# Kernel tuning notes

Hardware: AMD Instinct MI355X
Metric: run time of the kernel (lower is better)

The kernel has to match this reference:

```python
import jax, jax.numpy as jnp
import numpy as np

B, S, D = 4, 512, 4096
H, G = 32, 8           # num_heads, num_groups (GQA)
HD = D // H            # head_dim = 128
REP = H // G           # query heads per kv group = 4


def rotate_half(x):
    x1, x2 = x[..., : x.shape[-1] // 2], x[..., x.shape[-1] // 2 :]
    return jnp.concatenate([-x2, x1], axis=-1)


def setup_inputs() -> dict:
    key = jax.random.key(0)
    ks = jax.random.split(key, 5)
    return {
        "x": jax.random.normal(ks[0], (B, S, D), dtype=jnp.float32),
        "wq": jax.random.normal(ks[1], (D, D), dtype=jnp.float32) * 0.02,
        "bq": jnp.zeros((D,), dtype=jnp.float32),
        "wk": jax.random.normal(ks[2], (D, G * HD), dtype=jnp.float32) * 0.02,
        "bk": jnp.zeros((G * HD,), dtype=jnp.float32),
        "wv": jax.random.normal(ks[3], (D, G * HD), dtype=jnp.float32) * 0.02,
        "bv": jnp.zeros((G * HD,), dtype=jnp.float32),
        "wo": jax.random.normal(ks[4], (D, D), dtype=jnp.float32) * 0.02,
        "bo": jnp.zeros((D,), dtype=jnp.float32),
    }


def reference(x, wq, bq, wk, bk, wv, bv, wo, bo):
    b, s, d = x.shape
    q = (x @ wq + bq).reshape(b, s, H, HD)
    k = (x @ wk + bk).reshape(b, s, G, HD)
    v = (x @ wv + bv).reshape(b, s, G, HD)

    # RoPE tables (identical to module's cached sin/cos, sliced to seq len)
    inv_freq = 1.0 / (10000.0 ** (jnp.arange(0, HD, 2, dtype=jnp.float32) / HD))
    freqs = jnp.outer(jnp.arange(s, dtype=jnp.float32), inv_freq)  # [s, HD/2]
    freqs = jnp.concatenate([freqs, freqs], axis=-1)               # [s, HD]
    sin = jnp.sin(freqs)[:, None, :]  # [s, 1, HD] broadcast over heads
    cos = jnp.cos(freqs)[:, None, :]

    q = q * cos + rotate_half(q) * sin
    k = k * cos + rotate_half(k) * sin

    # Module scales q by HD**-0.5 AND jax.nn.dot_product_attention applies its
    # own default 1/sqrt(HD) -> net logit scale is HD**-1. Reproduce exactly.
    scale = HD ** (-0.5)
    q = q * scale

    # GQA without materializing repeated k/v: group query heads.
    qg = q.reshape(b, s, G, REP, HD)
    logits = jnp.einsum("bqgrd,bkgd->bgrqk", qg, k) * scale  # second scale (SDPA default)
    attn = jax.nn.softmax(logits, axis=-1)
    out = jnp.einsum("bgrqk,bkgd->bqgrd", attn, v).reshape(b, s, d)
    return out @ wo + bo
```

## Files before the change

kernel.cpp:

```cpp
#include <hip/hip_runtime.h>
#include <math.h>

typedef unsigned short ushort_t;
typedef __attribute__((ext_vector_type(8))) short bf16x8;
typedef __attribute__((ext_vector_type(4))) float f32x4;
typedef __attribute__((ext_vector_type(4))) unsigned short us4;
typedef __attribute__((ext_vector_type(8))) unsigned short us8;

#define B_   4
#define S_   512
#define D_   4096
#define H_   32
#define G_   8
#define HD_  128
#define KV_  1024
#define M_   (B_ * S_)
#define QN_  6144

__device__ __forceinline__ float bf2f(ushort_t u) {
    union { unsigned u; float f; } x; x.u = ((unsigned)u) << 16; return x.f;
}
__device__ __forceinline__ ushort_t f2bf(float f) {
    union { float f; unsigned u; } x; x.f = f;
    unsigned r = x.u + 0x7fffu + ((x.u >> 16) & 1u);
    return (ushort_t)(r >> 16);
}

typedef const __attribute__((address_space(1))) void* gptr_t;
typedef __attribute__((address_space(3))) void* ldsptr_t;

__device__ __forceinline__ void gload_lds16(const void* g, void* lds) {
    __builtin_amdgcn_global_load_lds((gptr_t)g, (ldsptr_t)lds, 16, 0, 0);
}

#define BAR() asm volatile("s_barrier" ::: "memory")
#define LGKM0() do { asm volatile("s_waitcnt lgkmcnt(0)" ::: "memory"); \
                     __builtin_amdgcn_sched_barrier(0); } while (0)

__global__ void xconv(const float* __restrict__ x, ushort_t* __restrict__ xb, int n8)
{
    const int i = blockIdx.x * blockDim.x + threadIdx.x;
    if (i >= n8) return;
    const float4 a = *(const float4*)&x[(size_t)i * 8];
    const float4 b = *(const float4*)&x[(size_t)i * 8 + 4];
    us8 o;
    o[0] = f2bf(a.x); o[1] = f2bf(a.y); o[2] = f2bf(a.z); o[3] = f2bf(a.w);
    o[4] = f2bf(b.x); o[5] = f2bf(b.y); o[6] = f2bf(b.z); o[7] = f2bf(b.w);
    *(us8*)&xb[(size_t)i * 8] = o;
}

__global__ __launch_bounds__(256) void wconv(
    const float* __restrict__ W, ushort_t* __restrict__ Wt, int K, int N)
{
    __shared__ float t[32][33];
    const int n0 = blockIdx.x * 32, k0 = blockIdx.y * 32;
    const int tid = threadIdx.x;
    const int r = tid >> 3, c4 = (tid & 7) * 4;
    const float4 v = *(const float4*)&W[(size_t)(k0 + r) * N + n0 + c4];
    t[r][c4 + 0] = v.x; t[r][c4 + 1] = v.y; t[r][c4 + 2] = v.z; t[r][c4 + 3] = v.w;
    __syncthreads();
    us4 o;
    o.x = f2bf(t[c4 + 0][r]);
    o.y = f2bf(t[c4 + 1][r]);
    o.z = f2bf(t[c4 + 2][r]);
    o.w = f2bf(t[c4 + 3][r]);
    *(us4*)&Wt[(size_t)(n0 + r) * K + k0 + c4] = o;
}

template<int OUT_BF16, int SPLITK>
__global__ __launch_bounds__(512, 2) void gemm8(
    const ushort_t* __restrict__ A, int lda,
    const ushort_t* __restrict__ Bt, int ldb,
    const float* __restrict__ bias0, const float* __restrict__ bias1,
    const float* __restrict__ bias2,
    float* __restrict__ Cf, ushort_t* __restrict__ Cb,
    float* __restrict__ P0, float* __restrict__ P1,
    int M, int N, int K)
{
    __shared__ ushort_t sA[2][256 * 64];
    __shared__ ushort_t sB[2][256 * 64];

    const int tid = threadIdx.x;
    const int lane = tid & 63, w = tid >> 6;
    const int lr = lane & 15, kg = lane >> 4;
    const int wr = w >> 2, wc = w & 3;

    const int nwg = gridDim.x;
    const int cpx = nwg >> 3;
    const int bid = (blockIdx.x & 7) * cpx + (blockIdx.x >> 3);
    int khalf = 0, tile = bid;
    if (SPLITK) { khalf = bid >> 7; tile = bid & 127; }
    const int nbx = N >> 8;
    const int bx = tile % nbx, by = tile / nbx;
    const int bm0 = by << 8, bn0 = bx << 8;
    if (SPLITK) { A += (size_t)khalf * K; Bt += (size_t)khalf * K; }

    const int NT = K >> 6;

    auto stage = [&](int t, int h) {
        const int c = t & 1;
        const ushort_t* gb; int ld; char* sbase;
        if (h < 2) { gb = A + (size_t)bm0 * lda; ld = lda; sbase = (char*)sA; }
        else       { gb = Bt + (size_t)bn0 * ldb; ld = ldb; sbase = (char*)sB; }
        const int half = h & 1;
        #pragma unroll
        for (int j = 0; j < 2; ++j) {
            const int o = j * 8192 + tid * 16;
            const int row = half * 128 + (o >> 7);
            const int slot = (o >> 4) & 7;
            gload_lds16(gb + (size_t)row * ld + t * 64 + ((slot ^ (row & 7)) << 3),
                        sbase + c * 32768 + half * 16384 + j * 8192 + w * 1024);
        }
    };
    auto lda_frag = [&](int c, int mi, int s) {
        const int row = mi * 32 + wr * 16 + lr;
        return *(const bf16x8*)((const char*)sA + c * 32768 + row * 128 +
                                (((s * 4 + kg) ^ (row & 7)) << 4));
    };
    auto ldb_frag = [&](int c, int ni, int s) {
        const int row = ni * 64 + wc * 16 + lr;
        return *(const bf16x8*)((const char*)sB + c * 32768 + row * 128 +
                                (((s * 4 + kg) ^ (row & 7)) << 4));
    };

    f32x4 acc[8][4];
    #pragma unroll
    for (int i = 0; i < 8; ++i)
        #pragma unroll
        for (int j = 0; j < 4; ++j)
            acc[i][j] = (f32x4){0.f, 0.f, 0.f, 0.f};

    stage(0, 0); stage(0, 2); stage(0, 3); stage(0, 1);
    stage(1, 0); stage(1, 2); stage(1, 3);
    asm volatile("s_waitcnt vmcnt(6)" ::: "memory");
    BAR();

    for (int t = 0; t < NT; ++t) {
        const int c = t & 1;
        bf16x8 a[4][2], b[4][2];

        #pragma unroll
        for (int mi = 0; mi < 4; ++mi)
            #pragma unroll
            for (int s = 0; s < 2; ++s) a[mi][s] = lda_frag(c, mi, s);
        #pragma unroll
        for (int ni = 0; ni < 2; ++ni)
            #pragma unroll
            for (int s = 0; s < 2; ++s) b[ni][s] = ldb_frag(c, ni, s);
        if (t + 1 < NT) stage(t + 1, 1);
        BAR();
        LGKM0();
        __builtin_amdgcn_s_setprio(1);
        #pragma unroll
        for (int mi = 0; mi < 4; ++mi)
            #pragma unroll
            for (int ni = 0; ni < 2; ++ni)
                #pragma unroll
                for (int s = 0; s < 2; ++s)
                    acc[mi][ni] = __builtin_amdgcn_mfma_f32_16x16x32_bf16(
                        a[mi][s], b[ni][s], acc[mi][ni], 0, 0, 0);
        __builtin_amdgcn_s_setprio(0);
        BAR();

        #pragma unroll
        for (int ni = 2; ni < 4; ++ni)
            #pragma unroll
            for (int s = 0; s < 2; ++s) b[ni][s] = ldb_frag(c, ni, s);
        if (t + 2 < NT) stage(t + 2, 0);
        BAR();
        LGKM0();
        __builtin_amdgcn_s_setprio(1);
        #pragma unroll
        for (int mi = 0; mi < 4; ++mi)
            #pragma unroll
            for (int ni = 2; ni < 4; ++ni)
                #pragma unroll
                for (int s = 0; s < 2; ++s)
                    acc[mi][ni] = __builtin_amdgcn_mfma_f32_16x16x32_bf16(
                        a[mi][s], b[ni][s], acc[mi][ni], 0, 0, 0);
        __builtin_amdgcn_s_setprio(0);
        BAR();

        #pragma unroll
        for (int mi = 0; mi < 4; ++mi)
            #pragma unroll
            for (int s = 0; s < 2; ++s) a[mi][s] = lda_frag(c, mi + 4, s);
        if (t + 2 < NT) stage(t + 2, 2);
        BAR();
        LGKM0();
        __builtin_amdgcn_s_setprio(1);
        #pragma unroll
        for (int mi = 0; mi < 4; ++mi)
            #pragma unroll
            for (int ni = 2; ni < 4; ++ni)
                #pragma unroll
                for (int s = 0; s < 2; ++s)
                    acc[mi + 4][ni] = __builtin_amdgcn_mfma_f32_16x16x32_bf16(
                        a[mi][s], b[ni][s], acc[mi + 4][ni], 0, 0, 0);
        __builtin_amdgcn_s_setprio(0);
        BAR();

        if (t + 2 < NT) {
            stage(t + 2, 3);
            asm volatile("s_waitcnt vmcnt(6)" ::: "memory");
        } else {
            asm volatile("s_waitcnt vmcnt(0)" ::: "memory");
        }
        BAR();
        __builtin_amdgcn_s_setprio(1);
        #pragma unroll
        for (int mi = 0; mi < 4; ++mi)
            #pragma unroll
            for (int ni = 0; ni < 2; ++ni)
                #pragma unroll
                for (int s = 0; s < 2; ++s)
                    acc[mi + 4][ni] = __builtin_amdgcn_mfma_f32_16x16x32_bf16(
                        a[mi][s], b[ni][s], acc[mi + 4][ni], 0, 0, 0);
        __builtin_amdgcn_s_setprio(0);
        BAR();
    }

    #pragma unroll
    for (int mi = 0; mi < 8; ++mi) {
        #pragma unroll
        for (int ni = 0; ni < 4; ++ni) {
            const int n = bn0 + ni * 64 + wc * 16 + lr;
            const float bs = (n < 4096) ? bias0[n]
                           : (n < 5120) ? bias1[n - 4096] : bias2[n - 5120];
            const int mr = bm0 + mi * 32 + wr * 16 + kg * 4;
            #pragma unroll
            for (int r = 0; r < 4; ++r) {
                if (SPLITK) {
                    const int row = mr + r;
                    if (khalf == 0) {
                        Cf[(size_t)row * N + n] = acc[mi][ni][r] + bs;
                    } else {
                        float* P = (row < 1024) ? P0 : P1;
                        P[((size_t)(row & 1023) << 12) + n] = acc[mi][ni][r];
                    }
                } else {
                    const float val = acc[mi][ni][r] + bs;
                    if (OUT_BF16) Cb[(size_t)(mr + r) * N + n] = f2bf(val);
                    else          Cf[(size_t)(mr + r) * N + n] = val;
                }
            }
        }
    }
}

__global__ void reduce_add(const float* __restrict__ P0, const float* __restrict__ P1,
                           float* __restrict__ out)
{
    const int i4 = blockIdx.x * blockDim.x + threadIdx.x;
    if (i4 >= M_ * D_ / 4) return;
    const float4 p = (i4 < (1 << 20))
        ? *(const float4*)&P0[(size_t)i4 * 4]
        : *(const float4*)&P1[(size_t)(i4 - (1 << 20)) * 4];
    float4 o = *(float4*)&out[(size_t)i4 * 4];
    o.x += p.x; o.y += p.y; o.z += p.z; o.w += p.w;
    *(float4*)&out[(size_t)i4 * 4] = o;
}

__global__ void rope_bf16(ushort_t* __restrict__ buf, int nh, float scale)
{
    const int i = blockIdx.x * blockDim.x + threadIdx.x;
    const int total = B_ * S_ * nh * 64;
    if (i >= total) return;
    const int j     = i & 63;
    const int t2    = i >> 6;
    const int head  = t2 % nh;
    const int token = t2 / nh;
    const int s     = token % S_;
    const size_t base = (size_t)token * QN_ + head * HD_;
    const float inv = __expf(-9.210340371976184f * (2.f * j) / (float)HD_);
    const float ang = (float)s * inv;
    float sn, cs;
    __sincosf(ang, &sn, &cs);
    const float x1 = bf2f(buf[base + j]);
    const float x2 = bf2f(buf[base + j + 64]);
    buf[base + j]      = f2bf((x1 * cs - x2 * sn) * scale);
    buf[base + j + 64] = f2bf((x2 * cs + x1 * sn) * scale);
}

__global__ __launch_bounds__(256) void vtrans(
    const ushort_t* __restrict__ vb,
    ushort_t* __restrict__ vT)
{
    __shared__ ushort_t t[32][40];
    const int s0 = blockIdx.x * 32;
    const int d0 = blockIdx.y * 32;
    const int bg = blockIdx.z;
    const int b = bg >> 3, g = bg & 7;
    const int tid = threadIdx.x;
    const int row = tid >> 3, c4 = (tid & 7) * 4;
    const us4 v = *(const us4*)&vb[(size_t)(b * S_ + s0 + row) * QN_ + g * HD_ + d0 + c4];
    t[row][c4 + 0] = v.x; t[row][c4 + 1] = v.y;
    t[row][c4 + 2] = v.z; t[row][c4 + 3] = v.w;
    __syncthreads();
    us4 o;
    o.x = t[c4 + 0][row]; o.y = t[c4 + 1][row];
    o.z = t[c4 + 2][row]; o.w = t[c4 + 3][row];
    *(us4*)&vT[(size_t)(bg * HD_ + d0 + row) * S_ + s0 + c4] = o;
}

__global__ __launch_bounds__(256) void attn_mfma(
    const ushort_t* __restrict__ kb,
    const ushort_t* __restrict__ vT,
    ushort_t* __restrict__ qb)
{
    __shared__ ushort_t sKV[8192];
    __shared__ ushort_t sP[4 * 16 * 512];

    const int q0 = blockIdx.x * 64;
    const int h = blockIdx.y, b = blockIdx.z;
    const int g = h >> 2;
    const int tid = threadIdx.x;
    const int lane = tid & 63, w = tid >> 6;
    const int lr = lane & 15, kg = lane >> 4;

    bf16x8 af[4];
    {
        const ushort_t* qrow = qb + (size_t)(b * S_ + q0 + w * 16 + lr) * QN_ + h * HD_;
        #pragma unroll
        for (int c = 0; c < 4; ++c)
            af[c] = *(const bf16x8*)(qrow + c * 32 + kg * 8);
    }

    f32x4 l[8][4];
    #pragma unroll
    for (int ch = 0; ch < 8; ++ch)
        #pragma unroll
        for (int t = 0; t < 4; ++t)
            l[ch][t] = (f32x4){0.f, 0.f, 0.f, 0.f};

    const ushort_t* kbase = kb + (size_t)b * S_ * QN_ + g * HD_;
    #pragma unroll
    for (int ch = 0; ch < 8; ++ch) {
        __syncthreads();
        #pragma unroll
        for (int i = 0; i < 4; ++i) {
            const int o = w * 4096 + i * 1024;
            const int key = (o >> 8) + (lane >> 4);
            const int sl = lane & 15;
            gload_lds16(kbase + (size_t)(ch * 64 + key) * QN_ + ((sl ^ (key & 15)) * 8),
                        (char*)sKV + o);
        }
        __syncthreads();
        #pragma unroll
        for (int t = 0; t < 4; ++t) {
            const int key = t * 16 + lr;
            #pragma unroll
            for (int c = 0; c < 4; ++c) {
                const bf16x8 bf = *(const bf16x8*)((const char*)sKV + key * 256 +
                                                   (((c * 4 + kg) ^ (key & 15)) << 4));
                l[ch][t] = __builtin_amdgcn_mfma_f32_16x16x32_bf16(af[c], bf, l[ch][t], 0, 0, 0);
            }
        }
    }

    float inv[4];
    #pragma unroll
    for (int r = 0; r < 4; ++r) {
        float m = -1e30f;
        #pragma unroll
        for (int ch = 0; ch < 8; ++ch)
            #pragma unroll
            for (int t = 0; t < 4; ++t)
                m = fmaxf(m, l[ch][t][r]);
        #pragma unroll
        for (int msk = 1; msk <= 8; msk <<= 1)
            m = fmaxf(m, __shfl_xor(m, msk));
        float s = 0.f;
        const int q = kg * 4 + r;
        #pragma unroll
        for (int ch = 0; ch < 8; ++ch)
            #pragma unroll
            for (int t = 0; t < 4; ++t) {
                const float p = __expf(l[ch][t][r] - m);
                s += p;
                const int gs = ch * 8 + t * 2 + (lr >> 3);
                sP[w * 8192 + q * 512 + ((gs ^ q) << 3) + (lr & 7)] = f2bf(p);
            }
        #pragma unroll
        for (int msk = 1; msk <= 8; msk <<= 1)
            s += __shfl_xor(s, msk);
        inv[r] = 1.f / s;
    }

    f32x4 oacc[8];
    #pragma unroll
    for (int dt = 0; dt < 8; ++dt) oacc[dt] = (f32x4){0.f, 0.f, 0.f, 0.f};

    const ushort_t* vbase = vT + (size_t)(b * G_ + g) * HD_ * S_;
    for (int ch = 0; ch < 8; ++ch) {
        __syncthreads();
        #pragma unroll
        for (int i = 0; i < 4; ++i) {
            const int o = w * 4096 + i * 1024;
            const int d = (o >> 7) + (lane >> 3);
            const int sl = lane & 7;
            gload_lds16(vbase + (size_t)d * S_ + ch * 64 + ((sl ^ (d & 7)) * 8),
                        (char*)sKV + o);
        }
        __syncthreads();
        #pragma unroll
        for (int c2 = 0; c2 < 2; ++c2) {
            const int gs = ch * 8 + c2 * 4 + kg;
            const bf16x8 ap = *(const bf16x8*)((const char*)sP + w * 16384 + lr * 1024 +
                                               ((gs ^ lr) << 4));
            #pragma unroll
            for (int dt = 0; dt < 8; ++dt) {
                const int d = dt * 16 + lr;
                const bf16x8 bv = *(const bf16x8*)((const char*)sKV + d * 128 +
                                                   (((c2 * 4 + kg) ^ (d & 7)) << 4));
                oacc[dt] = __builtin_amdgcn_mfma_f32_16x16x32_bf16(ap, bv, oacc[dt], 0, 0, 0);
            }
        }
    }

    #pragma unroll
    for (int dt = 0; dt < 8; ++dt) {
        #pragma unroll
        for (int r = 0; r < 4; ++r) {
            const int q = kg * 4 + r;
            qb[(size_t)(b * S_ + q0 + w * 16 + q) * QN_ + h * HD_ + dt * 16 + lr] =
                f2bf(oacc[dt][r] * inv[r]);
        }
    }
}

extern "C" void kernel_launch(void* const* d_in, const int* in_sizes, int n_in,
                              void* d_out, int out_size, void* d_ws, size_t ws_size,
                              hipStream_t stream)
{
    const float* x  = (const float*)d_in[0];
    const float* wq = (const float*)d_in[1];
    const float* bq = (const float*)d_in[2];
    const float* wk = (const float*)d_in[3];
    const float* bk = (const float*)d_in[4];
    const float* wv = (const float*)d_in[5];
    const float* bv = (const float*)d_in[6];
    const float* wo = (const float*)d_in[7];
    const float* bo = (const float*)d_in[8];
    float* out = (float*)d_out;

    char* ws = (char*)d_ws;
    ushort_t* xb   = (ushort_t*)(ws);
    ushort_t* Wt   = (ushort_t*)(ws + (16u << 20));
    ushort_t* vT   = (ushort_t*)(ws + (48u << 20));
    ushort_t* qkv  = (ushort_t*)(ws + (64u << 20));
    float* p0      = (float*)xb;
    float* p1      = (float*)(ws + (48u << 20));

    wconv<<<dim3(D_ / 32, D_ / 32), 256, 0, stream>>>(wq, Wt, D_, D_);
    wconv<<<dim3(KV_ / 32, D_ / 32), 256, 0, stream>>>(wk, Wt + (size_t)4096 * 4096, D_, KV_);
    wconv<<<dim3(KV_ / 32, D_ / 32), 256, 0, stream>>>(wv, Wt + (size_t)5120 * 4096, D_, KV_);
    xconv<<<(M_ * D_ / 8 + 255) / 256, 256, 0, stream>>>(x, xb, M_ * D_ / 8);

    gemm8<1, 0><<<(QN_ / 256) * (M_ / 256), 512, 0, stream>>>(
        xb, D_, Wt, D_, bq, bk, bv, nullptr, qkv, nullptr, nullptr, M_, QN_, D_);

    vtrans<<<dim3(S_ / 32, HD_ / 32, B_ * G_), 256, 0, stream>>>(qkv + 5120, vT);

    rope_bf16<<<(B_ * S_ * H_ * 64 + 255) / 256, 256, 0, stream>>>(qkv, H_, 1.f / 128.f);
    rope_bf16<<<(B_ * S_ * G_ * 64 + 255) / 256, 256, 0, stream>>>(qkv + 4096, G_, 1.f);

    attn_mfma<<<dim3(S_ / 64, H_, B_), 256, 0, stream>>>(qkv + 4096, vT, qkv);

    wconv<<<dim3(D_ / 32, D_ / 32), 256, 0, stream>>>(wo, Wt, D_, D_);

    gemm8<0, 1><<<256, 512, 0, stream>>>(
        qkv, QN_, Wt, D_, bo, bo, bo, out, nullptr, p0, p1, M_, D_, 2048);
    reduce_add<<<(M_ * D_ / 4 + 255) / 256, 256, 0, stream>>>(p0, p1, out);
}
```

Before: 327.0 us.

## Fuse RoPE into QKV GEMM epilogue and merge weight conversion launches

Applies rotary embedding and the q scaling directly in the QKV GEMM epilogue by pairing accumulator fragments 64 columns apart. This removes the two standalone rope kernels and their extra read-modify-write of q and k. The three weight-transpose conversions are merged into one launch, and reduce_add becomes a grid-stride loop with a fixed grid. The cost is extra sincos work and more register pressure in the GEMM epilogue.

```diff
diff --git a/kernel.cpp b/kernel.cpp
--- a/kernel.cpp
+++ b/kernel.cpp
@@ -47,6 +47,29 @@
     o[0] = f2bf(a.x); o[1] = f2bf(a.y); o[2] = f2bf(a.z); o[3] = f2bf(a.w);
     o[4] = f2bf(b.x); o[5] = f2bf(b.y); o[6] = f2bf(b.z); o[7] = f2bf(b.w);
     *(us8*)&xb[(size_t)i * 8] = o;
+}
+
+__global__ __launch_bounds__(256) void wconv_all(
+    const float* __restrict__ wq, const float* __restrict__ wk,
+    const float* __restrict__ wv, ushort_t* __restrict__ Wt)
+{
+    __shared__ float t[32][33];
+    const int n0 = blockIdx.x * 32, k0 = blockIdx.y * 32;
+    const float* W; int nsrc, N;
+    if (n0 < 4096)      { W = wq; nsrc = n0;        N = 4096; }
+    else if (n0 < 5120) { W = wk; nsrc = n0 - 4096; N = 1024; }
+    else                { W = wv; nsrc = n0 - 5120; N = 1024; }
+    const int tid = threadIdx.x;
+    const int r = tid >> 3, c4 = (tid & 7) * 4;
+    const float4 v = *(const float4*)&W[(size_t)(k0 + r) * N + nsrc + c4];
+    t[r][c4 + 0] = v.x; t[r][c4 + 1] = v.y; t[r][c4 + 2] = v.z; t[r][c4 + 3] = v.w;
+    __syncthreads();
+    us4 o;
+    o.x = f2bf(t[c4 + 0][r]);
+    o.y = f2bf(t[c4 + 1][r]);
+    o.z = f2bf(t[c4 + 2][r]);
+    o.w = f2bf(t[c4 + 3][r]);
+    *(us4*)&Wt[(size_t)(n0 + r) * D_ + k0 + c4] = o;
 }
 
 __global__ __launch_bounds__(256) void wconv(
@@ -67,7 +90,7 @@
     *(us4*)&Wt[(size_t)(n0 + r) * K + k0 + c4] = o;
 }
 
-template<int OUT_BF16, int SPLITK>
+template<int OUT_BF16, int SPLITK, int ROPE>
 __global__ __launch_bounds__(512, 2) void gemm8(
     const ushort_t* __restrict__ A, int lda,
     const ushort_t* __restrict__ Bt, int ldb,
@@ -220,6 +243,35 @@
         BAR();
     }
 
+    if (ROPE && bn0 < 5120) {
+        const float scale = (bn0 < 4096) ? (1.f / 128.f) : 1.f;
+        const int jj = wc * 16 + lr;
+        const float invf = __expf(-0.1439115683121279f * (float)jj);
+        #pragma unroll
+        for (int mi = 0; mi < 8; ++mi) {
+            const int mr = bm0 + mi * 32 + wr * 16 + kg * 4;
+            #pragma unroll
+            for (int r = 0; r < 4; ++r) {
+                const int srow = (mr + r) & 511;
+                float sn, cs;
+                __sincosf((float)srow * invf, &sn, &cs);
+                #pragma unroll
+                for (int nip = 0; nip < 2; ++nip) {
+                    const int n_lo = bn0 + nip * 128 + jj;
+                    const int n_hi = n_lo + 64;
+                    const float b_lo = (n_lo < 4096) ? bias0[n_lo]
+                                     : (n_lo < 5120) ? bias1[n_lo - 4096] : bias2[n_lo - 5120];
+                    const float b_hi = (n_hi < 4096) ? bias0[n_hi]
+                                     : (n_hi < 5120) ? bias1[n_hi - 4096] : bias2[n_hi - 5120];
+                    const float a_lo = acc[mi][nip * 2][r] + b_lo;
+                    const float a_hi = acc[mi][nip * 2 + 1][r] + b_hi;
+                    Cb[(size_t)(mr + r) * N + n_lo] = f2bf((a_lo * cs - a_hi * sn) * scale);
+                    Cb[(size_t)(mr + r) * N + n_hi] = f2bf((a_hi * cs + a_lo * sn) * scale);
+                }
+            }
+        }
+        return;
+    }
     #pragma unroll
     for (int mi = 0; mi < 8; ++mi) {
         #pragma unroll
@@ -251,35 +303,16 @@
 __global__ void reduce_add(const float* __restrict__ P0, const float* __restrict__ P1,
                            float* __restrict__ out)
 {
-    const int i4 = blockIdx.x * blockDim.x + threadIdx.x;
-    if (i4 >= M_ * D_ / 4) return;
-    const float4 p = (i4 < (1 << 20))
-        ? *(const float4*)&P0[(size_t)i4 * 4]
-        : *(const float4*)&P1[(size_t)(i4 - (1 << 20)) * 4];
-    float4 o = *(float4*)&out[(size_t)i4 * 4];
-    o.x += p.x; o.y += p.y; o.z += p.z; o.w += p.w;
-    *(float4*)&out[(size_t)i4 * 4] = o;
-}
-
-__global__ void rope_bf16(ushort_t* __restrict__ buf, int nh, float scale)
-{
-    const int i = blockIdx.x * blockDim.x + threadIdx.x;
-    const int total = B_ * S_ * nh * 64;
-    if (i >= total) return;
-    const int j     = i & 63;
-    const int t2    = i >> 6;
-    const int head  = t2 % nh;
-    const int token = t2 / nh;
-    const int s     = token % S_;
-    const size_t base = (size_t)token * QN_ + head * HD_;
-    const float inv = __expf(-9.210340371976184f * (2.f * j) / (float)HD_);
-    const float ang = (float)s * inv;
-    float sn, cs;
-    __sincosf(ang, &sn, &cs);
-    const float x1 = bf2f(buf[base + j]);
-    const float x2 = bf2f(buf[base + j + 64]);
-    buf[base + j]      = f2bf((x1 * cs - x2 * sn) * scale);
-    buf[base + j + 64] = f2bf((x2 * cs + x1 * sn) * scale);
+    const int n4 = M_ * D_ / 4;
+    for (int i4 = blockIdx.x * blockDim.x + threadIdx.x; i4 < n4;
+         i4 += gridDim.x * blockDim.x) {
+        const float4 p = (i4 < (1 << 20))
+            ? *(const float4*)&P0[(size_t)i4 * 4]
+            : *(const float4*)&P1[(size_t)(i4 - (1 << 20)) * 4];
+        float4 o = *(float4*)&out[(size_t)i4 * 4];
+        o.x += p.x; o.y += p.y; o.z += p.z; o.w += p.w;
+        *(float4*)&out[(size_t)i4 * 4] = o;
+    }
 }
 
 __global__ __launch_bounds__(256) void vtrans(
@@ -452,24 +485,19 @@
     float* p0      = (float*)xb;
     float* p1      = (float*)(ws + (48u << 20));
 
-    wconv<<<dim3(D_ / 32, D_ / 32), 256, 0, stream>>>(wq, Wt, D_, D_);
-    wconv<<<dim3(KV_ / 32, D_ / 32), 256, 0, stream>>>(wk, Wt + (size_t)4096 * 4096, D_, KV_);
-    wconv<<<dim3(KV_ / 32, D_ / 32), 256, 0, stream>>>(wv, Wt + (size_t)5120 * 4096, D_, KV_);
+    wconv_all<<<dim3(QN_ / 32, D_ / 32), 256, 0, stream>>>(wq, wk, wv, Wt);
     xconv<<<(M_ * D_ / 8 + 255) / 256, 256, 0, stream>>>(x, xb, M_ * D_ / 8);
 
-    gemm8<1, 0><<<(QN_ / 256) * (M_ / 256), 512, 0, stream>>>(
+    gemm8<1, 0, 1><<<(QN_ / 256) * (M_ / 256), 512, 0, stream>>>(
         xb, D_, Wt, D_, bq, bk, bv, nullptr, qkv, nullptr, nullptr, M_, QN_, D_);
 
     vtrans<<<dim3(S_ / 32, HD_ / 32, B_ * G_), 256, 0, stream>>>(qkv + 5120, vT);
 
-    rope_bf16<<<(B_ * S_ * H_ * 64 + 255) / 256, 256, 0, stream>>>(qkv, H_, 1.f / 128.f);
-    rope_bf16<<<(B_ * S_ * G_ * 64 + 255) / 256, 256, 0, stream>>>(qkv + 4096, G_, 1.f);
-
     attn_mfma<<<dim3(S_ / 64, H_, B_), 256, 0, stream>>>(qkv + 4096, vT, qkv);
 
     wconv<<<dim3(D_ / 32, D_ / 32), 256, 0, stream>>>(wo, Wt, D_, D_);
 
-    gemm8<0, 1><<<256, 512, 0, stream>>>(
+    gemm8<0, 1, 0><<<256, 512, 0, stream>>>(
         qkv, QN_, Wt, D_, bo, bo, bo, out, nullptr, p0, p1, M_, D_, 2048);
-    reduce_add<<<(M_ * D_ / 4 + 255) / 256, 256, 0, stream>>>(p0, p1, out);
-}
+    reduce_add<<<2048, 256, 0, stream>>>(p0, p1, out);
+}
```

After: 311.3 us. 4.8% less time.
